# Kernel tuning notes

Hardware: AMD Instinct MI355X
Metric: run time of the kernel (lower is better)

## Reference

```python
import jax, jax.numpy as jnp
import numpy as np

B, NN, S = 8, 511, 512          # graphs, nodes, seq (= nodes + graph token)
D, H, DH = 768, 12, 64          # hidden, heads, head dim
FFN, L = 3072, 6                # ffn size, layers
VOCAB = 512

def layer_norm(x, s, b, eps=1e-5):
    m = x.mean(-1, keepdims=True)
    v = ((x - m) ** 2).mean(-1, keepdims=True)
    return (x - m) / jnp.sqrt(v + eps) * s + b

def setup_inputs() -> dict:
    key = jax.random.key(0)
    ks = jax.random.split(key, 24)
    std = 0.02 / np.sqrt(L)
    inp = {}
    inp['attn_bias'] = jax.random.normal(ks[0], (B, S, S), jnp.float32) * 0.1
    inp['spatial_pos'] = jax.random.normal(ks[1], (B, NN, NN, 1), jnp.float32)
    inp['x'] = jax.random.randint(ks[2], (B, NN, 1), 0, VOCAB)
    node_emb = jax.random.normal(ks[3], (VOCAB, D), jnp.float32) * 0.02
    inp['node_emb'] = node_emb.at[0].set(0.0)  # padding_idx=0
    inp['graph_token'] = jax.random.normal(ks[4], (1, D), jnp.float32) * 0.02
    inp['virt_dist'] = jax.random.normal(ks[5], (1, H), jnp.float32) * 0.02
    inp['sp_w1'] = jax.random.normal(ks[6], (1, 128), jnp.float32) * std
    inp['sp_b1'] = jnp.zeros((128,), jnp.float32)
    inp['sp_w2'] = jax.random.normal(ks[7], (128, H), jnp.float32) * std
    inp['sp_b2'] = jnp.zeros((H,), jnp.float32)
    inp['ln1_s'] = jnp.ones((L, D), jnp.float32)
    inp['ln1_b'] = jnp.zeros((L, D), jnp.float32)
    inp['wq'] = jax.random.normal(ks[8], (L, D, D), jnp.float32) * std
    inp['bq'] = jnp.zeros((L, D), jnp.float32)
    inp['wk'] = jax.random.normal(ks[9], (L, D, D), jnp.float32) * std
    inp['bk'] = jnp.zeros((L, D), jnp.float32)
    inp['wv'] = jax.random.normal(ks[10], (L, D, D), jnp.float32) * std
    inp['bv'] = jnp.zeros((L, D), jnp.float32)
    inp['wo'] = jax.random.normal(ks[11], (L, D, D), jnp.float32) * std
    inp['bo'] = jnp.zeros((L, D), jnp.float32)
    inp['ln2_s'] = jnp.ones((L, D), jnp.float32)
    inp['ln2_b'] = jnp.zeros((L, D), jnp.float32)
    inp['fw1'] = jax.random.normal(ks[12], (L, D, FFN), jnp.float32) * std
    inp['fb1'] = jnp.zeros((L, FFN), jnp.float32)
    inp['fw2'] = jax.random.normal(ks[13], (L, FFN, D), jnp.float32) * std
    inp['fb2'] = jnp.zeros((L, D), jnp.float32)
    inp['fln_s'] = jnp.ones((D,), jnp.float32)
    inp['fln_b'] = jnp.zeros((D,), jnp.float32)
    return inp

def reference(attn_bias, spatial_pos, x, node_emb, graph_token, virt_dist,
              sp_w1, sp_b1, sp_w2, sp_b2,
              ln1_s, ln1_b, wq, bq, wk, bk, wv, bv, wo, bo,
              ln2_s, ln2_b, fw1, fb1, fw2, fb2, fln_s, fln_b):
    scale = DH ** -0.5
    # node features: embedding lookup summed over per-node feature indices
    h = node_emb[x].sum(axis=-2)                                   # [B, NN, D]
    h = jnp.concatenate([jnp.broadcast_to(graph_token[None], (B, 1, D)), h], axis=1)  # [B, S, D]
    # structural bias: spatial-pos MLP -> per-head bias on node block
    sp_bias = (spatial_pos @ sp_w1 + sp_b1) @ sp_w2 + sp_b2        # [B, NN, NN, H]
    sp_bias = sp_bias.transpose(0, 3, 1, 2)                         # [B, H, NN, NN]
    # original adds attn_bias twice (clone-repeat, then + attn_bias.unsqueeze(1))
    bias = jnp.broadcast_to((2.0 * attn_bias)[:, None], (B, H, S, S))
    t = virt_dist.reshape(1, H, 1)
    bias = bias.at[:, :, 1:, 1:].add(sp_bias)
    bias = bias.at[:, :, 1:, 0].add(t)
    bias = bias.at[:, :, 0, :].add(t)
    for l in range(L):
        y = layer_norm(h, ln1_s[l], ln1_b[l])
        q = (y @ wq[l] + bq[l]).reshape(B, S, H, DH) * scale
        k = (y @ wk[l] + bk[l]).reshape(B, S, H, DH)
        v = (y @ wv[l] + bv[l]).reshape(B, S, H, DH)
        scores = jnp.einsum('bihd,bjhd->bhij', q, k) + bias
        att = jax.nn.softmax(scores, axis=-1)
        o = jnp.einsum('bhij,bjhd->bihd', att, v).reshape(B, S, D)
        h = h + (o @ wo[l] + bo[l])
        y = layer_norm(h, ln2_s[l], ln2_b[l])
        h = h + (jax.nn.gelu(y @ fw1[l] + fb1[l], approximate=False) @ fw2[l] + fb2[l])
    return layer_norm(h, fln_s, fln_b)
```

## Files before the change

kernel.cpp:

```cpp
#include <hip/hip_runtime.h>
#include <cstdint>
#include <cstddef>


typedef __attribute__((ext_vector_type(8))) short bf16x8;
typedef __attribute__((ext_vector_type(4))) short bf16x4;
typedef __attribute__((ext_vector_type(4))) float f32x4;
typedef __attribute__((ext_vector_type(4))) unsigned int u32x4;

static constexpr int D    = 768;
static constexpr int H    = 12;
static constexpr int S    = 512;
static constexpr int NN   = 511;
static constexpr int B    = 8;
static constexpr int FFN  = 3072;
static constexpr int ROWS = B * S;

__device__ __forceinline__ short f2b(float x) {
    union { float f; uint32_t u; } c; c.f = x;
    uint32_t r = (c.u + 0x7fffu + ((c.u >> 16) & 1u)) >> 16;
    return (short)(uint16_t)r;
}
__device__ __forceinline__ float b2f_lo(uint32_t u) {
    union { uint32_t u; float f; } c; c.u = u << 16; return c.f;
}
__device__ __forceinline__ float b2f_hi(uint32_t u) {
    union { uint32_t u; float f; } c; c.u = u & 0xffff0000u; return c.f;
}
__device__ __forceinline__ float gelu_f(float x) {
    return 0.5f * x * (1.0f + erff(x * 0.7071067811865476f));
}
__device__ __forceinline__ void gload16(const void* g, void* l) {
    __builtin_amdgcn_global_load_lds(
        (const __attribute__((address_space(1))) void*)g,
        (__attribute__((address_space(3))) void*)l, 16, 0, 0);
}

#if __has_builtin(__builtin_amdgcn_mfma_f32_16x16x16bf16_1k)
__device__ __forceinline__ f32x4 mfma16(bf16x4 a, bf16x4 b, f32x4 c) {
    return __builtin_amdgcn_mfma_f32_16x16x16bf16_1k(a, b, c, 0, 0, 0);
}
__device__ __forceinline__ void mfma16_fence(f32x4* o) { (void)o; }
#else
__device__ __forceinline__ f32x4 mfma16(bf16x4 a, bf16x4 b, f32x4 c) {
    asm volatile("s_nop 1\n\tv_mfma_f32_16x16x16_bf16 %0, %1, %2, %0"
                 : "+v"(c) : "v"(a), "v"(b));
    return c;
}
__device__ __forceinline__ void mfma16_fence(f32x4* o) {
    asm volatile("s_nop 7\n\ts_nop 7"
                 : "+v"(o[0]), "+v"(o[1]), "+v"(o[2]), "+v"(o[3]));
}
#endif

__global__ __launch_bounds__(256) void embed_kernel(
    const int* __restrict__ x, const float* __restrict__ emb,
    const float* __restrict__ gtok, float* __restrict__ h)
{
    int row = blockIdx.x;
    int b = row >> 9, s = row & (S - 1);
    const float* src = (s == 0) ? gtok : (emb + (size_t)x[b * NN + (s - 1)] * D);
    float* dst = h + (size_t)row * D;
    int t = threadIdx.x;
    dst[t]       = src[t];
    dst[t + 256] = src[t + 256];
    dst[t + 512] = src[t + 512];
}

__global__ void ac_kernel(const float* __restrict__ w1, const float* __restrict__ b1,
                          const float* __restrict__ w2, const float* __restrict__ b2,
                          float* __restrict__ ac)
{
    int h = threadIdx.x;
    if (h < H) {
        float a = 0.f, c = 0.f;
        for (int k = 0; k < 128; ++k) { a += w1[k] * w2[k * H + h]; c += b1[k] * w2[k * H + h]; }
        ac[h] = a; ac[16 + h] = c + b2[h];
    }
}

__global__ __launch_bounds__(256) void bias_pack_kernel(
    const float* __restrict__ ab, const float* __restrict__ sp,
    uint32_t* __restrict__ pb)
{
    int row = blockIdx.x;
    int b = row >> 9, i = row & 511;
    const float* abr = ab + (size_t)row * S;
    const float* spr = sp + ((size_t)b * NN + (i - 1)) * NN;
    uint32_t* out = pb + (size_t)row * S;
    #pragma unroll
    for (int jt = 0; jt < 2; ++jt) {
        int j = jt * 256 + threadIdx.x;
        float a2 = 2.f * abr[j];
        float spv = (i > 0 && j > 0) ? spr[j - 1] : 0.f;
        out[j] = (uint32_t)(uint16_t)f2b(a2) | ((uint32_t)(uint16_t)f2b(spv) << 16);
    }
}

__global__ __launch_bounds__(256) void wcvt_kernel(
    const float* __restrict__ wq, const float* __restrict__ wk,
    const float* __restrict__ wv, const float* __restrict__ wo,
    const float* __restrict__ f1, const float* __restrict__ f2,
    short* __restrict__ wqkvT, short* __restrict__ woT,
    short* __restrict__ f1T, short* __restrict__ f2T)
{
    int t = blockIdx.x;
    const float* in; short* out; int R, C, tr, tc;
    if (t < 432) {
        int which = t / 144, tt = t - which * 144;
        in = (which == 0) ? wq : ((which == 1) ? wk : wv);
        out = wqkvT + (size_t)which * 768 * 768;
        R = 768; C = 768; tr = tt / 12; tc = tt % 12;
    } else if (t < 576) {
        int tt = t - 432; in = wo; out = woT; R = 768; C = 768; tr = tt / 12; tc = tt % 12;
    } else if (t < 1152) {
        int tt = t - 576; in = f1; out = f1T; R = 768; C = 3072; tr = tt / 48; tc = tt % 48;
    } else {
        int tt = t - 1152; in = f2; out = f2T; R = 3072; C = 768; tr = tt / 12; tc = tt % 12;
    }
    int r0 = tr * 64, c0 = tc * 64;
    __shared__ short tile[64][65];
    int tid = threadIdx.x;
    #pragma unroll
    for (int i = 0; i < 16; ++i) {
        int e = i * 256 + tid; int r = e >> 6, c = e & 63;
        tile[r][c] = f2b(in[(size_t)(r0 + r) * C + c0 + c]);
    }
    __syncthreads();
    #pragma unroll
    for (int i = 0; i < 16; ++i) {
        int e = i * 256 + tid; int c = e >> 6, r = e & 63;
        out[(size_t)(c0 + c) * R + r0 + r] = tile[r][c];
    }
}

__global__ __launch_bounds__(256) void ln_kernel(
    const float* __restrict__ in, const float* __restrict__ sc,
    const float* __restrict__ bi, float* __restrict__ outF,
    short* __restrict__ outB)
{
    int row = blockIdx.x, t = threadIdx.x;
    const float* x = in + (size_t)row * D;
    float e0 = x[t], e1 = x[t + 256], e2 = x[t + 512];
    float s  = e0 + e1 + e2;
    float sq = e0 * e0 + e1 * e1 + e2 * e2;
    #pragma unroll
    for (int off = 1; off < 64; off <<= 1) { s += __shfl_xor(s, off); sq += __shfl_xor(sq, off); }
    __shared__ float red[8];
    int w = t >> 6, lane = t & 63;
    if (lane == 0) { red[w] = s; red[4 + w] = sq; }
    __syncthreads();
    s  = red[0] + red[1] + red[2] + red[3];
    sq = red[4] + red[5] + red[6] + red[7];
    float m   = s * (1.f / D);
    float inv = rsqrtf(sq * (1.f / D) - m * m + 1e-5f);
    float v0 = (e0 - m) * inv * sc[t]       + bi[t];
    float v1 = (e1 - m) * inv * sc[t + 256] + bi[t + 256];
    float v2 = (e2 - m) * inv * sc[t + 512] + bi[t + 512];
    if (outB) {
        short* o = outB + (size_t)row * D;
        o[t] = f2b(v0); o[t + 256] = f2b(v1); o[t + 512] = f2b(v2);
    } else {
        float* o = outF + (size_t)row * D;
        o[t] = v0; o[t + 256] = v1; o[t + 512] = v2;
    }
}

template<int BM, int BN, int BK, bool NFAST>
__global__ __launch_bounds__(256) void gemm2(
    const short* __restrict__ A, const short* __restrict__ Wt,
    const float* __restrict__ Bb0, const float* __restrict__ Bb1, const float* __restrict__ Bb2,
    float* __restrict__ outF, const float* __restrict__ resid,
    short* __restrict__ outB,
    int K, int nper, int gx, float alpha0, int mode)
{
    constexpr int MR = BM / 32;
    constexpr int NR = BN / 32;
    constexpr int SUBK = BK / 32;
    constexpr int AU = BM * BK / 2048;
    constexpr int BU = BN * BK / 2048;
    constexpr int CH = BK / 8;
    constexpr int NL = AU + BU;
    __shared__ __align__(16) short As[3][BM * BK];
    __shared__ __align__(16) short Bs[3][BN * BK];
    int tid  = threadIdx.x;
    int lane = tid & 63;
    int w    = tid >> 6;

    int nwg = gridDim.x;
    int bid = blockIdx.x;
    int sid = (bid & 7) * (nwg >> 3) + (bid >> 3);
    int row0, n0;
    if (NFAST) { row0 = (sid / gx) * BM; n0 = (sid % gx) * BN; }
    else       { row0 = (sid % gx) * BM; n0 = (sid / gx) * BN; }

    int which = n0 / nper;
    int ncol0 = n0 - which * nper;
    const float* Bv = (which == 0) ? Bb0 : ((which == 1) ? Bb1 : Bb2);
    float alpha = (which == 0) ? alpha0 : 1.0f;

    int wr = (w >> 1) * (BM / 2);
    int wc = (w & 1) * (BN / 2);
    int fr = lane & 15;
    int q4 = lane >> 4;

    auto swz = [&](int r) -> int { return (BK == 64) ? (r & 7) : ((r >> 1) & 3); };

    f32x4 acc[MR][NR] = {};

    auto stageA = [&](int buf, int k0) {
        #pragma unroll
        for (int ii = 0; ii < AU; ++ii) {
            int U = ii * 256 + tid;
            int r = U / CH;
            int ch = (U % CH) ^ swz(r);
            gload16(A + (size_t)(row0 + r) * K + k0 + ch * 8,
                    (char*)&As[buf][0] + ((size_t)ii * 256 + w * 64) * 16);
        }
    };
    auto stageB = [&](int buf, int k0) {
        #pragma unroll
        for (int ii = 0; ii < BU; ++ii) {
            int U = ii * 256 + tid;
            int r = U / CH;
            int ch = (U % CH) ^ swz(r);
            gload16(Wt + (size_t)(n0 + r) * K + k0 + ch * 8,
                    (char*)&Bs[buf][0] + ((size_t)ii * 256 + w * 64) * 16);
        }
    };
    auto compute = [&](int buf) {
        #pragma unroll
        for (int s = 0; s < SUBK; ++s) {
            bf16x8 af[MR], bfr[NR];
            #pragma unroll
            for (int m = 0; m < MR; ++m) {
                int r = wr + m * 16 + fr;
                af[m] = *(const bf16x8*)((const char*)&As[buf][0]
                        + (size_t)r * (2 * BK) + (((q4 + 4 * s) ^ swz(r)) * 16));
            }
            #pragma unroll
            for (int n = 0; n < NR; ++n) {
                int r = wc + n * 16 + fr;
                bfr[n] = *(const bf16x8*)((const char*)&Bs[buf][0]
                        + (size_t)r * (2 * BK) + (((q4 + 4 * s) ^ swz(r)) * 16));
            }
            #pragma unroll
            for (int m = 0; m < MR; ++m)
                #pragma unroll
                for (int n = 0; n < NR; ++n)
                    acc[m][n] = __builtin_amdgcn_mfma_f32_16x16x32_bf16(af[m], bfr[n], acc[m][n], 0, 0, 0);
        }
    };

    int nt = K / BK;
    stageA(0, 0); stageB(0, 0);
    stageA(1, BK); stageB(1, BK);
    for (int t = 0; t < nt - 1; ++t) {
        asm volatile("s_waitcnt vmcnt(%0)" :: "i"(NL) : "memory");
        __builtin_amdgcn_sched_barrier(0);
        __builtin_amdgcn_s_barrier();
        if (t + 2 < nt) {
            int b2 = (t + 2) % 3;
            stageA(b2, (t + 2) * BK);
            stageB(b2, (t + 2) * BK);
        }
        compute(t % 3);
    }
    asm volatile("s_waitcnt vmcnt(0)" ::: "memory");
    __builtin_amdgcn_sched_barrier(0);
    __builtin_amdgcn_s_barrier();
    compute((nt - 1) % 3);

    int rr = q4 * 4;
    if (mode == 1) {
        short* base = outB + (size_t)which * ROWS * D;
        #pragma unroll
        for (int m = 0; m < MR; ++m) {
            int rowb = row0 + wr + m * 16 + rr;
            int b2 = rowb >> 9, s0 = rowb & 511;
            #pragma unroll
            for (int n = 0; n < NR; ++n) {
                int col = ncol0 + wc + n * 16 + fr;
                int h2 = col >> 6, d2 = col & 63;
                float bv = Bv[col];
                if (which == 2) {
                    bf16x4 pk;
                    #pragma unroll
                    for (int ri = 0; ri < 4; ++ri) pk[ri] = f2b(acc[m][n][ri] + bv);
                    *(bf16x4*)&base[(((size_t)b2 * H + h2) * 64 + d2) * 512 + s0] = pk;
                } else {
                    #pragma unroll
                    for (int ri = 0; ri < 4; ++ri)
                        base[(((size_t)b2 * H + h2) * 512 + (s0 + ri)) * 64 + d2] =
                            f2b((acc[m][n][ri] + bv) * alpha);
                }
            }
        }
        return;
    }

    #pragma unroll
    for (int m = 0; m < MR; ++m) {
        #pragma unroll
        for (int n = 0; n < NR; ++n) {
            int col  = ncol0 + wc + n * 16 + fr;
            float bv = Bv[col];
            #pragma unroll
            for (int ri = 0; ri < 4; ++ri) {
                int row = row0 + wr + m * 16 + rr + ri;
                size_t idx = (size_t)row * nper + col;
                float val = acc[m][n][ri] + bv;
                if (mode == 2) {
                    outB[idx] = f2b(gelu_f(val));
                } else {
                    outF[idx] = val + resid[idx];
                }
            }
        }
    }
}

__global__ __launch_bounds__(256) void attn_kernel(
    const short* __restrict__ qb, const short* __restrict__ kbuf,
    const short* __restrict__ vtb,
    const uint32_t* __restrict__ pb,
    const float* __restrict__ vd, const float* __restrict__ ac,
    short* __restrict__ o)
{
    __shared__ __align__(16) short Ks[2][64 * 64];
    __shared__ __align__(16) short Vs[2][64 * 64];
    int tid = threadIdx.x, lane = tid & 63, w = tid >> 6;
    int bid = blockIdx.x;
    int b    = bid & 7;
    int qblk = (bid >> 3) & 7;
    int hh   = bid >> 6;
    int fr = lane & 15, g16 = lane >> 4;
    int kb8 = g16 * 8, rr = g16 * 4;
    int i0 = qblk * 64 + w * 16;
    int i  = i0 + fr;

    const short* qp = qb   + ((size_t)(b * H + hh) * S) * 64;
    const short* kp = kbuf + ((size_t)(b * H + hh) * S) * 64;
    const short* vp = vtb  + ((size_t)(b * H + hh) * 64) * S;

    bf16x8 aq0 = *(const bf16x8*)&qp[(i0 + fr) * 64 + kb8];
    bf16x8 aq1 = *(const bf16x8*)&qp[(i0 + fr) * 64 + 32 + kb8];

    float Ah = ac[hh], Ch = ac[16 + hh], th = vd[hh];
    const uint32_t* pbb = pb + (size_t)b * S * S + (size_t)i * S;

    auto stageK = [&](int buf, int j0) {
        #pragma unroll
        for (int ii = 0; ii < 2; ++ii) {
            int U = ii * 256 + tid;
            int r = U >> 3;
            int ch = (U & 7) ^ (r & 7);
            gload16(kp + (size_t)(j0 + r) * 64 + ch * 8,
                    (char*)&Ks[buf][0] + ((size_t)ii * 256 + w * 64) * 16);
        }
    };
    auto stageV = [&](int buf, int j0) {
        #pragma unroll
        for (int ii = 0; ii < 2; ++ii) {
            int U = ii * 256 + tid;
            int d = U >> 3;
            int s8 = (2 * (U & 7)) ^ (d & 14);
            gload16(vp + (size_t)d * S + j0 + s8 * 4,
                    (char*)&Vs[buf][0] + ((size_t)ii * 256 + w * 64) * 16);
        }
    };

    float m_run = -3.0e38f, l_run = 0.f;
    f32x4 oacc[4] = {};

    stageK(0, 0);
    stageV(0, 0);
    __syncthreads();
    int buf = 0;
    #pragma unroll 1
    for (int t = 0; t < 8; ++t) {
        if (t < 7) { stageK(buf ^ 1, (t + 1) * 64); stageV(buf ^ 1, (t + 1) * 64); }
        f32x4 s[4];
        #pragma unroll
        for (int jt = 0; jt < 4; ++jt) {
            int jb = t * 4 + jt;
            u32x4 u = *(const u32x4*)&pbb[jb * 16 + rr];
            f32x4 c;
            #pragma unroll
            for (int ri = 0; ri < 4; ++ri) {
                int j = jb * 16 + rr + ri;
                float bias = b2f_lo(u[ri]);
                if (i > 0 && j > 0) bias += b2f_hi(u[ri]) * Ah + Ch;
                if (i == 0 || j == 0) bias += th;
                c[ri] = bias;
            }
            int r = jt * 16 + fr;
            const char* krow = (const char*)&Ks[buf][0] + r * 128;
            bf16x8 kf0 = *(const bf16x8*)(krow + ((g16 ^ (r & 7)) * 16));
            bf16x8 kf1 = *(const bf16x8*)(krow + (((g16 + 4) ^ (r & 7)) * 16));
            c = __builtin_amdgcn_mfma_f32_16x16x32_bf16(kf0, aq0, c, 0, 0, 0);
            s[jt] = __builtin_amdgcn_mfma_f32_16x16x32_bf16(kf1, aq1, c, 0, 0, 0);
        }
        float tm = s[0][0];
        #pragma unroll
        for (int jt = 0; jt < 4; ++jt)
            #pragma unroll
            for (int ri = 0; ri < 4; ++ri) tm = fmaxf(tm, s[jt][ri]);
        tm = fmaxf(tm, __shfl_xor(tm, 16));
        tm = fmaxf(tm, __shfl_xor(tm, 32));
        float mnew = fmaxf(m_run, tm);
        float scale = __expf(m_run - mnew);
        l_run *= scale;
        #pragma unroll
        for (int ri = 0; ri < 4; ++ri) {
            float scr = __shfl(scale, rr + ri);
            #pragma unroll
            for (int dt = 0; dt < 4; ++dt) oacc[dt][ri] *= scr;
        }
        #pragma unroll
        for (int jt = 0; jt < 4; ++jt)
            #pragma unroll
            for (int ri = 0; ri < 4; ++ri) {
                float p = __expf(s[jt][ri] - mnew);
                s[jt][ri] = p;
                l_run += p;
            }
        #pragma unroll
        for (int jt = 0; jt < 4; ++jt) {
            bf16x4 pa;
            #pragma unroll
            for (int ri = 0; ri < 4; ++ri) pa[ri] = f2b(s[jt][ri]);
            #pragma unroll
            for (int dt = 0; dt < 4; ++dt) {
                int d = dt * 16 + fr;
                const char* vrow = (const char*)&Vs[buf][0] + d * 128;
                bf16x4 vb = *(const bf16x4*)(vrow + (((jt * 4 + g16) ^ (d & 14)) * 8));
                oacc[dt] = mfma16(pa, vb, oacc[dt]);
            }
        }
        m_run = mnew;
        __syncthreads();
        buf ^= 1;
    }
    mfma16_fence(oacc);

    l_run += __shfl_xor(l_run, 16);
    l_run += __shfl_xor(l_run, 32);
    float invl = 1.f / l_run;
    #pragma unroll
    for (int ri = 0; ri < 4; ++ri) {
        float ivr = __shfl(invl, rr + ri);
        #pragma unroll
        for (int dt = 0; dt < 4; ++dt)
            o[((size_t)(b * S + i0 + rr + ri) * H + hh) * 64 + dt * 16 + fr] =
                f2b(oacc[dt][ri] * ivr);
    }
}

extern "C" void kernel_launch(void* const* d_in, const int* in_sizes, int n_in,
                              void* d_out, int out_size, void* d_ws, size_t ws_size,
                              hipStream_t stream)
{
    const float* attn_bias   = (const float*)d_in[0];
    const float* spatial_pos = (const float*)d_in[1];
    const int*   xx          = (const int*)d_in[2];
    const float* node_emb    = (const float*)d_in[3];
    const float* graph_token = (const float*)d_in[4];
    const float* virt_dist   = (const float*)d_in[5];
    const float* sp_w1 = (const float*)d_in[6];
    const float* sp_b1 = (const float*)d_in[7];
    const float* sp_w2 = (const float*)d_in[8];
    const float* sp_b2 = (const float*)d_in[9];
    const float* ln1_s = (const float*)d_in[10];
    const float* ln1_b = (const float*)d_in[11];
    const float* wq = (const float*)d_in[12];
    const float* bq = (const float*)d_in[13];
    const float* wk = (const float*)d_in[14];
    const float* bk = (const float*)d_in[15];
    const float* wv = (const float*)d_in[16];
    const float* bv = (const float*)d_in[17];
    const float* wo = (const float*)d_in[18];
    const float* bo = (const float*)d_in[19];
    const float* ln2_s = (const float*)d_in[20];
    const float* ln2_b = (const float*)d_in[21];
    const float* fw1 = (const float*)d_in[22];
    const float* fb1 = (const float*)d_in[23];
    const float* fw2 = (const float*)d_in[24];
    const float* fb2 = (const float*)d_in[25];
    const float* fln_s = (const float*)d_in[26];
    const float* fln_b = (const float*)d_in[27];

    float* wsf = (float*)d_ws;
    const size_t SZ = (size_t)ROWS * D;
    float* h   = wsf;
    float* acb = wsf + SZ;
    short* s16 = (short*)(wsf + SZ + 64);
    short* yob = s16;
    short* g16b = s16 + SZ;
    short* bfq = g16b + (size_t)ROWS * FFN;
    short* wqkvT = bfq + 3 * SZ;
    short* woT   = wqkvT + 2304 * 768;
    short* f1T   = woT + 768 * 768;
    short* f2T   = f1T + (size_t)3072 * 768;
    uint32_t* pbias = (uint32_t*)(f2T + (size_t)768 * 3072);

    embed_kernel<<<ROWS, 256, 0, stream>>>(xx, node_emb, graph_token, h);
    ac_kernel<<<1, 64, 0, stream>>>(sp_w1, sp_b1, sp_w2, sp_b2, acb);
    bias_pack_kernel<<<ROWS, 256, 0, stream>>>(attn_bias, spatial_pos, pbias);

    for (int l = 0; l < 6; ++l) {
        wcvt_kernel<<<1728, 256, 0, stream>>>(
            wq + (size_t)l * D * D, wk + (size_t)l * D * D, wv + (size_t)l * D * D,
            wo + (size_t)l * D * D, fw1 + (size_t)l * D * FFN, fw2 + (size_t)l * FFN * D,
            wqkvT, woT, f1T, f2T);
        ln_kernel<<<ROWS, 256, 0, stream>>>(h, ln1_s + l * D, ln1_b + l * D, nullptr, yob);
        gemm2<128, 128, 32, false><<<576, 256, 0, stream>>>(
            yob, wqkvT, bq + l * D, bk + l * D, bv + l * D,
            nullptr, nullptr, bfq, D, D, 32, 0.125f, 1);
        attn_kernel<<<B * H * 8, 256, 0, stream>>>(
            bfq, bfq + SZ, bfq + 2 * SZ, pbias, virt_dist, acb, yob);
        gemm2<64, 64, 64, true><<<768, 256, 0, stream>>>(
            yob, woT, bo + l * D, nullptr, nullptr,
            h, h, nullptr, D, D, 12, 1.0f, 0);
        ln_kernel<<<ROWS, 256, 0, stream>>>(h, ln2_s + l * D, ln2_b + l * D, nullptr, yob);
        gemm2<128, 128, 32, false><<<768, 256, 0, stream>>>(
            yob, f1T, fb1 + l * FFN, nullptr, nullptr,
            nullptr, nullptr, g16b, D, FFN, 32, 1.0f, 2);
        gemm2<64, 64, 64, true><<<768, 256, 0, stream>>>(
            g16b, f2T, fb2 + l * D, nullptr, nullptr,
            h, h, nullptr, FFN, D, 12, 1.0f, 0);
    }
    ln_kernel<<<ROWS, 256, 0, stream>>>(h, fln_s, fln_b, (float*)d_out, nullptr);
}
```

Before: 1.004 ms.

## Process two query tiles per attention block to reuse staged K/V

Each attention block now handles 128 query rows (two 64-row tiles per wave pair) instead of 64, so every K/V tile staged in shared memory feeds twice as many MFMAs. The grid is halved from 768 to 384 blocks. This is meant to cut global K/V traffic and staging overhead per unit of work. In exchange it doubles accumulator and score registers per thread, which can lower occupancy, and it leaves fewer blocks to fill the GPU's compute units.

```diff
diff --git a/kernel.cpp b/kernel.cpp
--- a/kernel.cpp
+++ b/kernel.cpp
@@ -332,22 +332,27 @@
     int tid = threadIdx.x, lane = tid & 63, w = tid >> 6;
     int bid = blockIdx.x;
     int b    = bid & 7;
-    int qblk = (bid >> 3) & 7;
-    int hh   = bid >> 6;
+    int qblk = (bid >> 3) & 3;
+    int hh   = bid >> 5;
     int fr = lane & 15, g16 = lane >> 4;
     int kb8 = g16 * 8, rr = g16 * 4;
-    int i0 = qblk * 64 + w * 16;
-    int i  = i0 + fr;
+    int i0A = qblk * 128 + w * 16;
+    int i0B = i0A + 64;
+    int iA  = i0A + fr;
+    int iB  = i0B + fr;
 
     const short* qp = qb   + ((size_t)(b * H + hh) * S) * 64;
     const short* kp = kbuf + ((size_t)(b * H + hh) * S) * 64;
     const short* vp = vtb  + ((size_t)(b * H + hh) * 64) * S;
 
-    bf16x8 aq0 = *(const bf16x8*)&qp[(i0 + fr) * 64 + kb8];
-    bf16x8 aq1 = *(const bf16x8*)&qp[(i0 + fr) * 64 + 32 + kb8];
+    bf16x8 aqA0 = *(const bf16x8*)&qp[(i0A + fr) * 64 + kb8];
+    bf16x8 aqA1 = *(const bf16x8*)&qp[(i0A + fr) * 64 + 32 + kb8];
+    bf16x8 aqB0 = *(const bf16x8*)&qp[(i0B + fr) * 64 + kb8];
+    bf16x8 aqB1 = *(const bf16x8*)&qp[(i0B + fr) * 64 + 32 + kb8];
 
     float Ah = ac[hh], Ch = ac[16 + hh], th = vd[hh];
-    const uint32_t* pbb = pb + (size_t)b * S * S + (size_t)i * S;
+    const uint32_t* pbbA = pb + (size_t)b * S * S + (size_t)iA * S;
+    const uint32_t* pbbB = pb + (size_t)b * S * S + (size_t)iB * S;
 
     auto stageK = [&](int buf, int j0) {
         #pragma unroll
@@ -370,8 +375,10 @@
         }
     };
 
-    float m_run = -3.0e38f, l_run = 0.f;
-    f32x4 oacc[4] = {};
+    float mA = -3.0e38f, lA = 0.f;
+    float mB = -3.0e38f, lB = 0.f;
+    f32x4 oaccA[4] = {};
+    f32x4 oaccB[4] = {};
 
     stageK(0, 0);
     stageV(0, 0);
@@ -380,80 +387,125 @@
     #pragma unroll 1
     for (int t = 0; t < 8; ++t) {
         if (t < 7) { stageK(buf ^ 1, (t + 1) * 64); stageV(buf ^ 1, (t + 1) * 64); }
-        f32x4 s[4];
+        f32x4 sA[4], sB[4];
         #pragma unroll
         for (int jt = 0; jt < 4; ++jt) {
             int jb = t * 4 + jt;
-            u32x4 u = *(const u32x4*)&pbb[jb * 16 + rr];
-            f32x4 c;
+            u32x4 uA = *(const u32x4*)&pbbA[jb * 16 + rr];
+            u32x4 uB = *(const u32x4*)&pbbB[jb * 16 + rr];
+            f32x4 cA, cB;
             #pragma unroll
             for (int ri = 0; ri < 4; ++ri) {
                 int j = jb * 16 + rr + ri;
-                float bias = b2f_lo(u[ri]);
-                if (i > 0 && j > 0) bias += b2f_hi(u[ri]) * Ah + Ch;
-                if (i == 0 || j == 0) bias += th;
-                c[ri] = bias;
+                float biasA = b2f_lo(uA[ri]);
+                if (iA > 0 && j > 0) biasA += b2f_hi(uA[ri]) * Ah + Ch;
+                if (iA == 0 || j == 0) biasA += th;
+                cA[ri] = biasA;
+                float biasB = b2f_lo(uB[ri]);
+                if (j > 0) biasB += b2f_hi(uB[ri]) * Ah + Ch;
+                if (j == 0) biasB += th;
+                cB[ri] = biasB;
             }
             int r = jt * 16 + fr;
             const char* krow = (const char*)&Ks[buf][0] + r * 128;
             bf16x8 kf0 = *(const bf16x8*)(krow + ((g16 ^ (r & 7)) * 16));
             bf16x8 kf1 = *(const bf16x8*)(krow + (((g16 + 4) ^ (r & 7)) * 16));
-            c = __builtin_amdgcn_mfma_f32_16x16x32_bf16(kf0, aq0, c, 0, 0, 0);
-            s[jt] = __builtin_amdgcn_mfma_f32_16x16x32_bf16(kf1, aq1, c, 0, 0, 0);
-        }
-        float tm = s[0][0];
-        #pragma unroll
-        for (int jt = 0; jt < 4; ++jt)
-            #pragma unroll
-            for (int ri = 0; ri < 4; ++ri) tm = fmaxf(tm, s[jt][ri]);
-        tm = fmaxf(tm, __shfl_xor(tm, 16));
-        tm = fmaxf(tm, __shfl_xor(tm, 32));
-        float mnew = fmaxf(m_run, tm);
-        float scale = __expf(m_run - mnew);
-        l_run *= scale;
-        #pragma unroll
-        for (int ri = 0; ri < 4; ++ri) {
-            float scr = __shfl(scale, rr + ri);
-            #pragma unroll
-            for (int dt = 0; dt < 4; ++dt) oacc[dt][ri] *= scr;
-        }
-        #pragma unroll
-        for (int jt = 0; jt < 4; ++jt)
+            cA = __builtin_amdgcn_mfma_f32_16x16x32_bf16(kf0, aqA0, cA, 0, 0, 0);
+            sA[jt] = __builtin_amdgcn_mfma_f32_16x16x32_bf16(kf1, aqA1, cA, 0, 0, 0);
+            cB = __builtin_amdgcn_mfma_f32_16x16x32_bf16(kf0, aqB0, cB, 0, 0, 0);
+            sB[jt] = __builtin_amdgcn_mfma_f32_16x16x32_bf16(kf1, aqB1, cB, 0, 0, 0);
+        }
+        {
+            float tm = sA[0][0];
+            #pragma unroll
+            for (int jt = 0; jt < 4; ++jt)
+                #pragma unroll
+                for (int ri = 0; ri < 4; ++ri) tm = fmaxf(tm, sA[jt][ri]);
+            tm = fmaxf(tm, __shfl_xor(tm, 16));
+            tm = fmaxf(tm, __shfl_xor(tm, 32));
+            float mnew = fmaxf(mA, tm);
+            float scale = __expf(mA - mnew);
+            lA *= scale;
             #pragma unroll
             for (int ri = 0; ri < 4; ++ri) {
-                float p = __expf(s[jt][ri] - mnew);
-                s[jt][ri] = p;
-                l_run += p;
-            }
+                float scr = __shfl(scale, rr + ri);
+                #pragma unroll
+                for (int dt = 0; dt < 4; ++dt) oaccA[dt][ri] *= scr;
+            }
+            #pragma unroll
+            for (int jt = 0; jt < 4; ++jt)
+                #pragma unroll
+                for (int ri = 0; ri < 4; ++ri) {
+                    float p = __expf(sA[jt][ri] - mnew);
+                    sA[jt][ri] = p;
+                    lA += p;
+                }
+            mA = mnew;
+        }
+        {
+            float tm = sB[0][0];
+            #pragma unroll
+            for (int jt = 0; jt < 4; ++jt)
+                #pragma unroll
+                for (int ri = 0; ri < 4; ++ri) tm = fmaxf(tm, sB[jt][ri]);
+            tm = fmaxf(tm, __shfl_xor(tm, 16));
+            tm = fmaxf(tm, __shfl_xor(tm, 32));
+            float mnew = fmaxf(mB, tm);
+            float scale = __expf(mB - mnew);
+            lB *= scale;
+            #pragma unroll
+            for (int ri = 0; ri < 4; ++ri) {
+                float scr = __shfl(scale, rr + ri);
+                #pragma unroll
+                for (int dt = 0; dt < 4; ++dt) oaccB[dt][ri] *= scr;
+            }
+            #pragma unroll
+            for (int jt = 0; jt < 4; ++jt)
+                #pragma unroll
+                for (int ri = 0; ri < 4; ++ri) {
+                    float p = __expf(sB[jt][ri] - mnew);
+                    sB[jt][ri] = p;
+                    lB += p;
+                }
+            mB = mnew;
+        }
         #pragma unroll
         for (int jt = 0; jt < 4; ++jt) {
-            bf16x4 pa;
-            #pragma unroll
-            for (int ri = 0; ri < 4; ++ri) pa[ri] = f2b(s[jt][ri]);
+            bf16x4 paA, paB;
+            #pragma unroll
+            for (int ri = 0; ri < 4; ++ri) { paA[ri] = f2b(sA[jt][ri]); paB[ri] = f2b(sB[jt][ri]); }
             #pragma unroll
             for (int dt = 0; dt < 4; ++dt) {
                 int d = dt * 16 + fr;
                 const char* vrow = (const char*)&Vs[buf][0] + d * 128;
                 bf16x4 vb = *(const bf16x4*)(vrow + (((jt * 4 + g16) ^ (d & 14)) * 8));
-                oacc[dt] = mfma16(pa, vb, oacc[dt]);
-            }
-        }
-        m_run = mnew;
+                oaccA[dt] = mfma16(paA, vb, oaccA[dt]);
+                oaccB[dt] = mfma16(paB, vb, oaccB[dt]);
+            }
+        }
         __syncthreads();
         buf ^= 1;
     }
-    mfma16_fence(oacc);
-
-    l_run += __shfl_xor(l_run, 16);
-    l_run += __shfl_xor(l_run, 32);
-    float invl = 1.f / l_run;
+    mfma16_fence(oaccA);
+    mfma16_fence(oaccB);
+
+    lA += __shfl_xor(lA, 16);
+    lA += __shfl_xor(lA, 32);
+    lB += __shfl_xor(lB, 16);
+    lB += __shfl_xor(lB, 32);
+    float invlA = 1.f / lA;
+    float invlB = 1.f / lB;
     #pragma unroll
     for (int ri = 0; ri < 4; ++ri) {
-        float ivr = __shfl(invl, rr + ri);
-        #pragma unroll
-        for (int dt = 0; dt < 4; ++dt)
-            o[((size_t)(b * S + i0 + rr + ri) * H + hh) * 64 + dt * 16 + fr] =
-                f2b(oacc[dt][ri] * ivr);
+        float ivA = __shfl(invlA, rr + ri);
+        float ivB = __shfl(invlB, rr + ri);
+        #pragma unroll
+        for (int dt = 0; dt < 4; ++dt) {
+            o[((size_t)(b * S + i0A + rr + ri) * H + hh) * 64 + dt * 16 + fr] =
+                f2b(oaccA[dt][ri] * ivA);
+            o[((size_t)(b * S + i0B + rr + ri) * H + hh) * 64 + dt * 16 + fr] =
+                f2b(oaccB[dt][ri] * ivB);
+        }
     }
 }
 
@@ -517,7 +569,7 @@
         gemm2<128, 128, 32, false><<<576, 256, 0, stream>>>(
             yob, wqkvT, bq + l * D, bk + l * D, bv + l * D,
             nullptr, nullptr, bfq, D, D, 32, 0.125f, 1);
-        attn_kernel<<<B * H * 8, 256, 0, stream>>>(
+        attn_kernel<<<384, 256, 0, stream>>>(
             bfq, bfq + SZ, bfq + 2 * SZ, pbias, virt_dist, acb, yob);
         gemm2<64, 64, 64, true><<<768, 256, 0, stream>>>(
             yob, woT, bo + l * D, nullptr, nullptr,
```

New measurement: 1.031 ms. 1.03x slower.
